# Kernel tuning notes

Measured on AMD Instinct MI355X. Metric: run time of the kernel, lower is better.

Reference implementation:

```python
import jax, jax.numpy as jnp
import numpy as np

B, F, NB, E = 32768, 64, 64, 32


def setup_inputs() -> dict:
    key = jax.random.key(0)
    k1, k2, k3, k4 = jax.random.split(key, 4)
    x = jax.random.normal(k1, (B, F), dtype=jnp.float32)
    # per-feature sorted bin edges (as produced by PLE.adapt quantiles)
    bins = jnp.sort(jax.random.uniform(k2, (F, NB), dtype=jnp.float32,
                                       minval=-2.0, maxval=2.0), axis=1)
    W = jax.random.normal(k3, (F, NB, E), dtype=jnp.float32) / np.sqrt(NB)
    b = jax.random.normal(k4, (F, E), dtype=jnp.float32)
    return {"x": x, "bins": bins, "W": W, "b": b}


def reference(x, bins, W, b):
    # x: [B,F], bins: [F,NB] sorted edges, W: [F,NB,E], b: [F,E]
    nb = bins.shape[1]
    lo = bins  # bins[j] == lookup_table[i-1] for bin i=j+1
    # lookup_table.get(i, -1): last bin has no upper edge -> defaults to -1.0
    hi = jnp.concatenate(
        [bins[:, 1:], jnp.full((bins.shape[0], 1), -1.0, bins.dtype)], axis=1)
    j = jnp.arange(nb)
    xe = x[:, :, None]                                  # [B,F,1]
    left = (xe < lo[None]) & (j > 0)                    # [B,F,NB]
    right = (xe >= hi[None]) & (j < nb - 1)             # [B,F,NB]
    v = (xe - lo[None]) / (hi - lo)[None]               # interpolation value
    # enc = 0 where left, 1 where neither, v where exactly one of left/right
    enc = jnp.where(left != right, v, jnp.where(left, 0.0, 1.0))  # [B,F,NB]
    # per-feature linear + ReLU, then features stacked along dim 1
    emb = jax.nn.relu(jnp.einsum('bfn,fne->bfe', enc, W) + b[None])  # [B,F,E]
    return emb
```

## Files before the change

### kernel.cpp

```cpp
#include <hip/hip_runtime.h>


#define FDIM 64
#define NB   64
#define EDIM 32
#define BT   16

typedef __attribute__((ext_vector_type(4))) float f32x4;

__global__ __launch_bounds__(256) void prep_kernel(
    const float* __restrict__ bins, const float* __restrict__ W,
    const float* __restrict__ bias,
    float* __restrict__ P, float* __restrict__ R)
{
    const int f = blockIdx.x;
    const int t = threadIdx.x;
    __shared__ float sg[NB];
    __shared__ float sb[NB];
    __shared__ float redP[8][EDIM];
    __shared__ float redQ[8][EDIM];

    if (t < NB) {
        float lo = bins[f * NB + t];
        float hi = (t < NB - 1) ? bins[f * NB + t + 1] : -1.0f;
        sg[t] = 1.0f / (hi - lo);
        sb[t] = lo;
    }
    __syncthreads();

    const int e  = t & (EDIM - 1);
    const int ch = t >> 5;
    float p = 0.0f, q = 0.0f;
    const float* Wf = W + (size_t)f * NB * EDIM + e;
    #pragma unroll
    for (int i = 0; i < 8; ++i) {
        int n = ch * 8 + i;
        float w = Wf[n * EDIM];
        p = fmaf(sg[n], w, p);
        q = fmaf(sb[n] * sg[n], w, q);
    }
    redP[ch][e] = p;
    redQ[ch][e] = q;
    __syncthreads();

    if (t < EDIM) {
        float P_ = 0.0f, Q_ = 0.0f;
        #pragma unroll
        for (int c = 0; c < 8; ++c) { P_ += redP[c][t]; Q_ += redQ[c][t]; }
        P[f * EDIM + t] = P_;
        R[f * EDIM + t] = bias[f * EDIM + t] - Q_;
    }
}

__global__ __launch_bounds__(256) void nemb_kernel(
    const float* __restrict__ x, const float* __restrict__ bins,
    const float* __restrict__ W,
    const float* __restrict__ P, const float* __restrict__ R,
    float* __restrict__ out)
{
    __shared__ float sBins[FDIM * (NB + 1)];
    __shared__ float sX[BT * FDIM];
    __shared__ float sC[BT * FDIM];
    __shared__ int   sK[BT * FDIM];

    const int t  = threadIdx.x;
    const long b0 = (long)blockIdx.x * BT;

    #pragma unroll
    for (int i = 0; i < 4; ++i) {
        int li = i * 256 + t;
        f32x4 v = reinterpret_cast<const f32x4*>(bins)[li];
        int el = li * 4;
        int f = el >> 6, n = el & 63;
        float* d = &sBins[f * (NB + 1) + n];
        d[0] = v.x; d[1] = v.y; d[2] = v.z; d[3] = v.w;
    }
    if (t < FDIM) sBins[t * (NB + 1) + NB] = -1.0f;
    reinterpret_cast<f32x4*>(sX)[t] =
        __builtin_nontemporal_load(reinterpret_cast<const f32x4*>(x + b0 * FDIM) + t);

    const int fA = t >> 3;
    const int fB = 32 + (t >> 3);
    const int e0 = (t & 7) * 4;
    const f32x4 PA = *reinterpret_cast<const f32x4*>(P + fA * EDIM + e0);
    const f32x4 RA = *reinterpret_cast<const f32x4*>(R + fA * EDIM + e0);
    const f32x4 PB = *reinterpret_cast<const f32x4*>(P + fB * EDIM + e0);
    const f32x4 RB = *reinterpret_cast<const f32x4*>(R + fB * EDIM + e0);

    __syncthreads();

    {
        const int f2  = t & 63;
        const int bi0 = t >> 6;
        const float* bl = &sBins[f2 * (NB + 1)];
        #pragma unroll
        for (int i = 0; i < 4; ++i) {
            int bi = bi0 + 4 * i;
            float xv = sX[bi * FDIM + f2];
            int k = (bl[32] <= xv) ? 32 : 0;
            if (bl[k + 16] <= xv) k += 16;
            if (bl[k +  8] <= xv) k +=  8;
            if (bl[k +  4] <= xv) k +=  4;
            if (bl[k +  2] <= xv) k +=  2;
            if (bl[k +  1] <= xv) k +=  1;
            float lo = bl[k];
            float hi = bl[k + 1];
            float c  = (hi - xv) * __builtin_amdgcn_rcpf(hi - lo);
            sC[bi * FDIM + f2] = c;
            sK[bi * FDIM + f2] = k;
        }
    }
    __syncthreads();

    float* ob = out + b0 * (FDIM * EDIM);
    f32x4 wA[2][4], wB[2][4];

    #pragma unroll
    for (int j = 0; j < 4; ++j) {
        int kA = sK[j * FDIM + fA];
        int kB = sK[j * FDIM + fB];
        wA[0][j] = *reinterpret_cast<const f32x4*>(W + ((fA * NB + kA) * EDIM) + e0);
        wB[0][j] = *reinterpret_cast<const f32x4*>(W + ((fB * NB + kB) * EDIM) + e0);
    }

    #pragma unroll
    for (int q = 0; q < 4; ++q) {
        const int cur = q & 1, nxt = cur ^ 1;
        if (q < 3) {
            #pragma unroll
            for (int j = 0; j < 4; ++j) {
                int bi = (q + 1) * 4 + j;
                int kA = sK[bi * FDIM + fA];
                int kB = sK[bi * FDIM + fB];
                wA[nxt][j] = *reinterpret_cast<const f32x4*>(W + ((fA * NB + kA) * EDIM) + e0);
                wB[nxt][j] = *reinterpret_cast<const f32x4*>(W + ((fB * NB + kB) * EDIM) + e0);
            }
        }
        #pragma unroll
        for (int j = 0; j < 4; ++j) {
            int bi = q * 4 + j;
            float xAv = sX[bi * FDIM + fA];
            float cAv = sC[bi * FDIM + fA];
            float xBv = sX[bi * FDIM + fB];
            float cBv = sC[bi * FDIM + fB];
            f32x4 oA, oB;
            oA.x = fmaxf(fmaf(cAv, wA[cur][j].x, fmaf(xAv, PA.x, RA.x)), 0.0f);
            oA.y = fmaxf(fmaf(cAv, wA[cur][j].y, fmaf(xAv, PA.y, RA.y)), 0.0f);
            oA.z = fmaxf(fmaf(cAv, wA[cur][j].z, fmaf(xAv, PA.z, RA.z)), 0.0f);
            oA.w = fmaxf(fmaf(cAv, wA[cur][j].w, fmaf(xAv, PA.w, RA.w)), 0.0f);
            oB.x = fmaxf(fmaf(cBv, wB[cur][j].x, fmaf(xBv, PB.x, RB.x)), 0.0f);
            oB.y = fmaxf(fmaf(cBv, wB[cur][j].y, fmaf(xBv, PB.y, RB.y)), 0.0f);
            oB.z = fmaxf(fmaf(cBv, wB[cur][j].z, fmaf(xBv, PB.z, RB.z)), 0.0f);
            oB.w = fmaxf(fmaf(cBv, wB[cur][j].w, fmaf(xBv, PB.w, RB.w)), 0.0f);

            f32x4* orow = reinterpret_cast<f32x4*>(ob + (long)bi * (FDIM * EDIM));
            orow[t]       = oA;
            orow[256 + t] = oB;
        }
    }
}

extern "C" void kernel_launch(void* const* d_in, const int* in_sizes, int n_in,
                              void* d_out, int out_size, void* d_ws, size_t ws_size,
                              hipStream_t stream) {
    const float* x    = (const float*)d_in[0];
    const float* bins = (const float*)d_in[1];
    const float* W    = (const float*)d_in[2];
    const float* bias = (const float*)d_in[3];
    float* out = (float*)d_out;

    float* P = (float*)d_ws;
    float* R = P + FDIM * EDIM;

    const int B = in_sizes[0] / FDIM;

    prep_kernel<<<FDIM, 256, 0, stream>>>(bins, W, bias, P, R);
    nemb_kernel<<<B / BT, 256, 0, stream>>>(x, bins, W, P, R, out);
}
```

Baseline: 61.62 us.

## Make each wavefront own four rows to drop the block barrier after binning

Each wavefront now loads x for its own four batch rows, runs the bin search in registers and stores x, interpolation coefficient and bin index to a private LDS region with a swizzled column offset. A wave-local lgkmcnt wait replaces the second __syncthreads. The output loop then walks features per wave, reloading P and R per feature and removing the double-buffered W prefetch. This cuts block-wide synchronisation and staging, but gives up explicit prefetching of the gathered W rows.

```diff
diff --git a/kernel.cpp b/kernel.cpp
--- a/kernel.cpp
+++ b/kernel.cpp
@@ -4,9 +4,9 @@
 #define FDIM 64
 #define NB   64
 #define EDIM 32
-#define BT   16
 
 typedef __attribute__((ext_vector_type(4))) float f32x4;
+typedef __attribute__((ext_vector_type(4))) int   i32x4;
 
 __global__ __launch_bounds__(256) void prep_kernel(
     const float* __restrict__ bins, const float* __restrict__ W,
@@ -59,12 +59,11 @@
     float* __restrict__ out)
 {
     __shared__ float sBins[FDIM * (NB + 1)];
-    __shared__ float sX[BT * FDIM];
-    __shared__ float sC[BT * FDIM];
-    __shared__ int   sK[BT * FDIM];
+    __shared__ float sX[16 * 64];
+    __shared__ float sC[16 * 64];
+    __shared__ int   sK[16 * 64];
 
-    const int t  = threadIdx.x;
-    const long b0 = (long)blockIdx.x * BT;
+    const int t = threadIdx.x;
 
     #pragma unroll
     for (int i = 0; i < 4; ++i) {
@@ -76,86 +75,68 @@
         d[0] = v.x; d[1] = v.y; d[2] = v.z; d[3] = v.w;
     }
     if (t < FDIM) sBins[t * (NB + 1) + NB] = -1.0f;
-    reinterpret_cast<f32x4*>(sX)[t] =
-        __builtin_nontemporal_load(reinterpret_cast<const f32x4*>(x + b0 * FDIM) + t);
-
-    const int fA = t >> 3;
-    const int fB = 32 + (t >> 3);
-    const int e0 = (t & 7) * 4;
-    const f32x4 PA = *reinterpret_cast<const f32x4*>(P + fA * EDIM + e0);
-    const f32x4 RA = *reinterpret_cast<const f32x4*>(R + fA * EDIM + e0);
-    const f32x4 PB = *reinterpret_cast<const f32x4*>(P + fB * EDIM + e0);
-    const f32x4 RB = *reinterpret_cast<const f32x4*>(R + fB * EDIM + e0);
-
     __syncthreads();
 
-    {
-        const int f2  = t & 63;
-        const int bi0 = t >> 6;
-        const float* bl = &sBins[f2 * (NB + 1)];
-        #pragma unroll
-        for (int i = 0; i < 4; ++i) {
-            int bi = bi0 + 4 * i;
-            float xv = sX[bi * FDIM + f2];
-            int k = (bl[32] <= xv) ? 32 : 0;
-            if (bl[k + 16] <= xv) k += 16;
-            if (bl[k +  8] <= xv) k +=  8;
-            if (bl[k +  4] <= xv) k +=  4;
-            if (bl[k +  2] <= xv) k +=  2;
-            if (bl[k +  1] <= xv) k +=  1;
-            float lo = bl[k];
-            float hi = bl[k + 1];
-            float c  = (hi - xv) * __builtin_amdgcn_rcpf(hi - lo);
-            sC[bi * FDIM + f2] = c;
-            sK[bi * FDIM + f2] = k;
-        }
-    }
-    __syncthreads();
+    const int w  = t >> 6;
+    const int l  = t & 63;
+    const int u  = l >> 4;
+    const int m  = l & 15;
+    const int d8 = l >> 3;
+    const int e0 = (l & 7) * 4;
+    const long g = (long)blockIdx.x * 4 + w;
+    const int prow = w * 4;
 
-    float* ob = out + b0 * (FDIM * EDIM);
-    f32x4 wA[2][4], wB[2][4];
+    f32x4 x4 = __builtin_nontemporal_load(
+        reinterpret_cast<const f32x4*>(x + (4 * g + u) * FDIM + 4 * m));
 
+    float cc[4]; int kk[4];
     #pragma unroll
     for (int j = 0; j < 4; ++j) {
-        int kA = sK[j * FDIM + fA];
-        int kB = sK[j * FDIM + fB];
-        wA[0][j] = *reinterpret_cast<const f32x4*>(W + ((fA * NB + kA) * EDIM) + e0);
-        wB[0][j] = *reinterpret_cast<const f32x4*>(W + ((fB * NB + kB) * EDIM) + e0);
+        const float* bl = &sBins[(4 * m + j) * (NB + 1)];
+        float xv = x4[j];
+        int k = (bl[32] <= xv) ? 32 : 0;
+        if (bl[k + 16] <= xv) k += 16;
+        if (bl[k +  8] <= xv) k +=  8;
+        if (bl[k +  4] <= xv) k +=  4;
+        if (bl[k +  2] <= xv) k +=  2;
+        if (bl[k +  1] <= xv) k +=  1;
+        float lo = bl[k];
+        float hi = bl[k + 1];
+        cc[j] = (hi - xv) * __builtin_amdgcn_rcpf(hi - lo);
+        kk[j] = k;
     }
 
+    {
+        int wbase = (prow + u) * 64 + ((4 * m + 8 * u) & 63);
+        *reinterpret_cast<f32x4*>(&sX[wbase]) = x4;
+        f32x4 cv4; cv4.x = cc[0]; cv4.y = cc[1]; cv4.z = cc[2]; cv4.w = cc[3];
+        *reinterpret_cast<f32x4*>(&sC[wbase]) = cv4;
+        i32x4 kv4; kv4.x = kk[0]; kv4.y = kk[1]; kv4.z = kk[2]; kv4.w = kk[3];
+        *reinterpret_cast<i32x4*>(&sK[wbase]) = kv4;
+    }
+    asm volatile("s_waitcnt lgkmcnt(0)" ::: "memory");
+
+    float* og = out + (4 * g) * (FDIM * EDIM);
     #pragma unroll
-    for (int q = 0; q < 4; ++q) {
-        const int cur = q & 1, nxt = cur ^ 1;
-        if (q < 3) {
-            #pragma unroll
-            for (int j = 0; j < 4; ++j) {
-                int bi = (q + 1) * 4 + j;
-                int kA = sK[bi * FDIM + fA];
-                int kB = sK[bi * FDIM + fB];
-                wA[nxt][j] = *reinterpret_cast<const f32x4*>(W + ((fA * NB + kA) * EDIM) + e0);
-                wB[nxt][j] = *reinterpret_cast<const f32x4*>(W + ((fB * NB + kB) * EDIM) + e0);
-            }
-        }
+    for (int i = 0; i < 8; ++i) {
+        const int fi = 8 * i + d8;
+        f32x4 Pv = *reinterpret_cast<const f32x4*>(P + fi * EDIM + e0);
+        f32x4 Rv = *reinterpret_cast<const f32x4*>(R + fi * EDIM + e0);
         #pragma unroll
-        for (int j = 0; j < 4; ++j) {
-            int bi = q * 4 + j;
-            float xAv = sX[bi * FDIM + fA];
-            float cAv = sC[bi * FDIM + fA];
-            float xBv = sX[bi * FDIM + fB];
-            float cBv = sC[bi * FDIM + fB];
-            f32x4 oA, oB;
-            oA.x = fmaxf(fmaf(cAv, wA[cur][j].x, fmaf(xAv, PA.x, RA.x)), 0.0f);
-            oA.y = fmaxf(fmaf(cAv, wA[cur][j].y, fmaf(xAv, PA.y, RA.y)), 0.0f);
-            oA.z = fmaxf(fmaf(cAv, wA[cur][j].z, fmaf(xAv, PA.z, RA.z)), 0.0f);
-            oA.w = fmaxf(fmaf(cAv, wA[cur][j].w, fmaf(xAv, PA.w, RA.w)), 0.0f);
-            oB.x = fmaxf(fmaf(cBv, wB[cur][j].x, fmaf(xBv, PB.x, RB.x)), 0.0f);
-            oB.y = fmaxf(fmaf(cBv, wB[cur][j].y, fmaf(xBv, PB.y, RB.y)), 0.0f);
-            oB.z = fmaxf(fmaf(cBv, wB[cur][j].z, fmaf(xBv, PB.z, RB.z)), 0.0f);
-            oB.w = fmaxf(fmaf(cBv, wB[cur][j].w, fmaf(xBv, PB.w, RB.w)), 0.0f);
-
-            f32x4* orow = reinterpret_cast<f32x4*>(ob + (long)bi * (FDIM * EDIM));
-            orow[t]       = oA;
-            orow[256 + t] = oB;
+        for (int r = 0; r < 4; ++r) {
+            int idx = (prow + r) * 64 + ((fi + 8 * r) & 63);
+            float xv = sX[idx];
+            float cv = sC[idx];
+            int   kv = sK[idx];
+            f32x4 Wv = *reinterpret_cast<const f32x4*>(
+                W + ((fi * NB + kv) * EDIM) + e0);
+            f32x4 o;
+            o.x = fmaxf(fmaf(cv, Wv.x, fmaf(xv, Pv.x, Rv.x)), 0.0f);
+            o.y = fmaxf(fmaf(cv, Wv.y, fmaf(xv, Pv.y, Rv.y)), 0.0f);
+            o.z = fmaxf(fmaf(cv, Wv.z, fmaf(xv, Pv.z, Rv.z)), 0.0f);
+            o.w = fmaxf(fmaf(cv, Wv.w, fmaf(xv, Pv.w, Rv.w)), 0.0f);
+            *reinterpret_cast<f32x4*>(og + (long)r * (FDIM * EDIM)
+                                      + fi * EDIM + e0) = o;
         }
     }
 }
@@ -175,5 +156,5 @@
     const int B = in_sizes[0] / FDIM;
 
     prep_kernel<<<FDIM, 256, 0, stream>>>(bins, W, bias, P, R);
-    nemb_kernel<<<B / BT, 256, 0, stream>>>(x, bins, W, P, R, out);
+    nemb_kernel<<<B / 16, 256, 0, stream>>>(x, bins, W, P, R, out);
 }
```

New measurement: 62.10 us. No clear change (+0.8%).
